# Performance work log

Hardware: AMD Instinct MI355X
Metric: run time of the kernel (lower is better)

Reference implementation:

```python
import jax, jax.numpy as jnp
import numpy as np
from jax import lax

FS, DW, CIN, COUT, NCLS, BATCH = 128, 8, 64, 256, 2, 512
K1, S1 = FS // 4, FS // 8          # 32, 16
L = FS * DW                        # 1024
T = (L - K1) // S1 + 1             # 63 SNN timesteps
BN_EPS = 1e-5


@jax.custom_vjp
def spike(u):
    """Heaviside spike on (v - threshold); surrogate grad exp(-|u|) (tau_grad=scale_grad=1)."""
    return (u >= 0).astype(u.dtype)

def _spike_fwd(u):
    return (u >= 0).astype(u.dtype), u

def _spike_bwd(u, g):
    return (g * jnp.exp(-jnp.abs(u)),)

spike.defvjp(_spike_fwd, _spike_bwd)


def cuba(x, threshold, current_decay, voltage_decay):
    """CUBA LIF scan. x: [N,C,T] -> binary spikes [N,C,T].
    i[t] = (1-cd)*i[t-1] + x[t]; v[t] = (1-vd)*v[t-1] + i[t]; s = v>=theta; v *= (1-s)."""
    cd, vd = 1.0 - current_decay, 1.0 - voltage_decay
    xs = jnp.moveaxis(x, -1, 0)  # [T,N,C]
    zero = jnp.zeros(x.shape[:-1], x.dtype)

    def step(carry, xt):
        i, v = carry
        i = cd * i + xt
        v = vd * v + i
        s = spike(v - threshold)
        v = v * (1.0 - s)
        return (i, v), s

    _, s = lax.scan(step, (zero, zero), xs)
    return jnp.moveaxis(s, 0, -1)


def conv1d(x, w, b, stride, pad):
    y = lax.conv_general_dilated(x, w, (stride,), [(pad, pad)],
                                 dimension_numbers=('NCH', 'OIH', 'NCH'))
    return y + b[None, :, None]


def bn(x, g, b, m, v):
    scale = g / jnp.sqrt(v + BN_EPS)
    return (x - m[None, :, None]) * scale[None, :, None] + b[None, :, None]


def setup_inputs() -> dict:
    key = jax.random.key(0)
    ks = jax.random.split(key, 12)
    return {
        'x':       jax.random.normal(ks[0], (BATCH, CIN, L), jnp.float32),
        'conv1_w': jax.random.normal(ks[1], (COUT, CIN, K1), jnp.float32) * 0.05,
        'conv1_b': jax.random.normal(ks[2], (COUT,), jnp.float32) * 0.05,
        'bn1_g':   jax.random.uniform(ks[3], (COUT,), jnp.float32, 0.5, 1.5),
        'bn1_b':   jax.random.normal(ks[4], (COUT,), jnp.float32) * 0.1,
        'bn1_m':   jax.random.normal(ks[5], (COUT,), jnp.float32) * 0.1,
        'bn1_v':   jax.random.uniform(ks[6], (COUT,), jnp.float32, 0.5, 1.5),
        'conv2_w': jax.random.normal(ks[7], (COUT, COUT, 3), jnp.float32) * 0.05,
        'conv2_b': jax.random.normal(ks[8], (COUT,), jnp.float32) * 0.05,
        'bn2_g':   jax.random.uniform(ks[9], (COUT,), jnp.float32, 0.5, 1.5),
        'bn2_b':   jax.random.normal(ks[10], (COUT,), jnp.float32) * 0.1,
        'bn2_m':   jax.random.normal(ks[11], (COUT,), jnp.float32) * 0.1,
        'bn2_v':   jax.random.uniform(jax.random.fold_in(key, 100), (COUT,), jnp.float32, 0.5, 1.5),
        'w1':      jax.random.normal(jax.random.fold_in(key, 101), (COUT, COUT), jnp.float32) * 0.1,
        'w2':      jax.random.normal(jax.random.fold_in(key, 102), (NCLS, COUT), jnp.float32) * 0.1,
    }


def reference(x, conv1_w, conv1_b, bn1_g, bn1_b, bn1_m, bn1_v,
              conv2_w, conv2_b, bn2_g, bn2_b, bn2_m, bn2_v, w1, w2):
    # CNN frontend (eval mode: BN uses running stats, dropout is identity)
    z = bn(conv1d(x, conv1_w, conv1_b, S1, 0), bn1_g, bn1_b, bn1_m, bn1_v)   # [N,COUT,T]
    z = bn(conv1d(z, conv2_w, conv2_b, 1, 1), bn2_g, bn2_b, bn2_m, bn2_v)    # [N,COUT,T]
    # CUBA Input encoder block: threshold=0.3, current_decay=0.9, voltage_decay=0.9
    z = cuba(z, 0.3, 0.9, 0.9)
    # CUBA Dense blocks (bias-free synapse per timestep + LIF): threshold=0.1, cd=1, vd=0.1
    z = cuba(jnp.einsum('oc,nct->not', w1, z), 0.1, 1.0, 0.1)
    z = cuba(jnp.einsum('oc,nct->not', w2, z), 0.1, 1.0, 0.1)
    return z  # binary spike trains [N, n_classes, T]
```

## Files before the change

kernel.cpp:

```cpp
#include <hip/hip_runtime.h>
#include <cstdint>
#include <cstddef>


typedef _Float16 half8 __attribute__((ext_vector_type(8)));
typedef float floatx4 __attribute__((ext_vector_type(4)));

__device__ __forceinline__ void split_f32(float v, _Float16& hi, _Float16& lo) {
    _Float16 h = (_Float16)v;
    hi = h;
    lo = (_Float16)((v - (float)h) * 2048.0f);
}

__global__ __launch_bounds__(256) void prep_kernel(
    const float* __restrict__ c1w, const float* __restrict__ c1b,
    const float* __restrict__ g1,  const float* __restrict__ b1,
    const float* __restrict__ m1,  const float* __restrict__ v1,
    const float* __restrict__ c2w, const float* __restrict__ c2b,
    const float* __restrict__ g2,  const float* __restrict__ b2,
    const float* __restrict__ m2,  const float* __restrict__ v2,
    const float* __restrict__ w1,
    _Float16* __restrict__ w1h, _Float16* __restrict__ w1l,
    _Float16* __restrict__ w2h, _Float16* __restrict__ w2l,
    _Float16* __restrict__ wdh, _Float16* __restrict__ wdl,
    float* __restrict__ ab1, float* __restrict__ ab2)
{
    const int id = blockIdx.x * 256 + threadIdx.x;
    if (id < 256) {
        float a1 = g1[id] / sqrtf(v1[id] + 1e-5f);
        ab1[id]       = a1;
        ab1[256 + id] = (c1b[id] - m1[id]) * a1 + b1[id];
        float a2 = g2[id] / sqrtf(v2[id] + 1e-5f);
        ab2[id]       = a2;
        ab2[256 + id] = (c2b[id] - m2[id]) * a2 + b2[id];
    }
    split_f32(w1[id], wdh[id], wdl[id]);
    for (int idx = id; idx < 256 * 2048; idx += 65536)
        split_f32(c1w[idx], w1h[idx], w1l[idx]);
    for (int idx = id; idx < 256 * 768; idx += 65536) {
        const int o  = idx / 768;
        const int r  = idx - o * 768;
        const int dt = r >> 8;
        const int c  = r & 255;
        split_f32(c2w[o * 768 + c * 3 + dt], w2h[idx], w2l[idx]);
    }
}

__global__ __launch_bounds__(256, 2) void conv1_mfma(
    const float* __restrict__ x,
    const _Float16* __restrict__ w1h, const _Float16* __restrict__ w1l,
    const float* __restrict__ ab,
    _Float16* __restrict__ z1h, _Float16* __restrict__ z1l)
{
    __shared__ _Float16 Ah[4][128][8];
    __shared__ _Float16 Al[4][128][8];
    __shared__ _Float16 Bh[4][128][8];
    __shared__ _Float16 Bl[4][128][8];

    const int tid = threadIdx.x;
    const int bm = blockIdx.x, bn = blockIdx.y;
    const int lr = tid & 127;
    const int h  = tid >> 7;

    const int am = bm * 128 + lr;
    const int an = am / 63, at = am - an * 63;
    const float*    arow  = x   + (size_t)an * 65536 + at * 16 + h * 16;
    const _Float16* bhrow = w1h + (size_t)(bn * 128 + lr) * 2048 + h * 16;
    const _Float16* blrow = w1l + (size_t)(bn * 128 + lr) * 2048 + h * 16;

    const int lane = tid & 63;
    const int wv   = tid >> 6;
    const int mw   = wv & 1, nw = wv >> 1;
    const int quad = lane >> 4;
    const int l15  = lane & 15;

    floatx4 accA[4][4] = {};
    floatx4 accB[4][4] = {};

    for (int it = 0; it < 64; ++it) {
        const float* ap = arow + it * 1024;
        float va[16];
        *(float4*)&va[0]  = *(const float4*)(ap);
        *(float4*)&va[4]  = *(const float4*)(ap + 4);
        *(float4*)&va[8]  = *(const float4*)(ap + 8);
        *(float4*)&va[12] = *(const float4*)(ap + 12);
        int4 bh0 = *(const int4*)(bhrow + it * 32);
        int4 bh1 = *(const int4*)(bhrow + it * 32 + 8);
        int4 bl0 = *(const int4*)(blrow + it * 32);
        int4 bl1 = *(const int4*)(blrow + it * 32 + 8);

        union U { _Float16 hf[8]; int4 v; };
        U c0h, c0l, c1h, c1l;
#pragma unroll
        for (int j = 0; j < 8; ++j) split_f32(va[j],     c0h.hf[j], c0l.hf[j]);
#pragma unroll
        for (int j = 0; j < 8; ++j) split_f32(va[8 + j], c1h.hf[j], c1l.hf[j]);

        __syncthreads();
        *(int4*)&Ah[2*h  ][lr][0] = c0h.v;
        *(int4*)&Ah[2*h+1][lr][0] = c1h.v;
        *(int4*)&Al[2*h  ][lr][0] = c0l.v;
        *(int4*)&Al[2*h+1][lr][0] = c1l.v;
        *(int4*)&Bh[2*h  ][lr][0] = bh0;
        *(int4*)&Bh[2*h+1][lr][0] = bh1;
        *(int4*)&Bl[2*h  ][lr][0] = bl0;
        *(int4*)&Bl[2*h+1][lr][0] = bl1;
        __syncthreads();

        half8 fah[4], fal[4], fbh[4], fbl[4];
#pragma unroll
        for (int t = 0; t < 4; ++t) {
            fah[t] = *(const half8*)&Ah[quad][mw*64 + t*16 + l15][0];
            fal[t] = *(const half8*)&Al[quad][mw*64 + t*16 + l15][0];
            fbh[t] = *(const half8*)&Bh[quad][nw*64 + t*16 + l15][0];
            fbl[t] = *(const half8*)&Bl[quad][nw*64 + t*16 + l15][0];
        }
#pragma unroll
        for (int ti = 0; ti < 4; ++ti)
#pragma unroll
            for (int tj = 0; tj < 4; ++tj) {
                accA[ti][tj] = __builtin_amdgcn_mfma_f32_16x16x32_f16(fah[ti], fbh[tj], accA[ti][tj], 0, 0, 0);
                accB[ti][tj] = __builtin_amdgcn_mfma_f32_16x16x32_f16(fah[ti], fbl[tj], accB[ti][tj], 0, 0, 0);
                accB[ti][tj] = __builtin_amdgcn_mfma_f32_16x16x32_f16(fal[ti], fbh[tj], accB[ti][tj], 0, 0, 0);
            }
    }

#pragma unroll
    for (int tj = 0; tj < 4; ++tj) {
        const int o = bn*128 + nw*64 + tj*16 + l15;
        const float alpha = ab[o], beta = ab[256 + o];
#pragma unroll
        for (int ti = 0; ti < 4; ++ti) {
            const int m0 = bm*128 + mw*64 + ti*16 + quad*4;
#pragma unroll
            for (int r = 0; r < 4; ++r) {
                float c = accA[ti][tj][r] + accB[ti][tj][r] * (1.0f/2048.0f);
                float z = c * alpha + beta;
                _Float16 zh, zl;
                split_f32(z, zh, zl);
                const size_t off = (size_t)(m0 + r) * 256 + o;
                z1h[off] = zh;
                z1l[off] = zl;
            }
        }
    }
}

__global__ __launch_bounds__(256, 2) void conv2_mfma(
    const _Float16* __restrict__ z1h, const _Float16* __restrict__ z1l,
    const _Float16* __restrict__ w2h, const _Float16* __restrict__ w2l,
    const float* __restrict__ ab, float* __restrict__ z2)
{
    __shared__ _Float16 Ah[4][128][8];
    __shared__ _Float16 Al[4][128][8];
    __shared__ _Float16 Bh[4][128][8];
    __shared__ _Float16 Bl[4][128][8];

    const int tid = threadIdx.x;
    const int bm = blockIdx.x, bn = blockIdx.y;
    const int lr = tid & 127;
    const int h  = tid >> 7;

    const int am = bm * 128 + lr;
    const int an = am / 63, at = am - an * 63;
    const _Float16* abase_h = z1h + (size_t)an * 16128;
    const _Float16* abase_l = z1l + (size_t)an * 16128;
    const _Float16* bhrow = w2h + (size_t)(bn * 128 + lr) * 768 + h * 16;
    const _Float16* blrow = w2l + (size_t)(bn * 128 + lr) * 768 + h * 16;

    const int lane = tid & 63;
    const int wv   = tid >> 6;
    const int mw   = wv & 1, nw = wv >> 1;
    const int quad = lane >> 4;
    const int l15  = lane & 15;

    floatx4 accA[4][4] = {};
    floatx4 accB[4][4] = {};

    const int4 z4 = {0, 0, 0, 0};

    for (int it = 0; it < 24; ++it) {
        const int kap0 = it * 32;
        const int dt   = kap0 >> 8;
        const int c0   = kap0 & 255;
        const int trow = at + dt - 1;
        const bool valid = (trow >= 0) && (trow < 63);
        const _Float16* aph = abase_h + trow * 256 + c0 + h * 16;
        const _Float16* apl = abase_l + trow * 256 + c0 + h * 16;
        int4 a0h = valid ? *(const int4*)(aph)     : z4;
        int4 a1h = valid ? *(const int4*)(aph + 8) : z4;
        int4 a0l = valid ? *(const int4*)(apl)     : z4;
        int4 a1l = valid ? *(const int4*)(apl + 8) : z4;
        int4 b0h = *(const int4*)(bhrow + kap0);
        int4 b1h = *(const int4*)(bhrow + kap0 + 8);
        int4 b0l = *(const int4*)(blrow + kap0);
        int4 b1l = *(const int4*)(blrow + kap0 + 8);

        __syncthreads();
        *(int4*)&Ah[2*h  ][lr][0] = a0h;
        *(int4*)&Ah[2*h+1][lr][0] = a1h;
        *(int4*)&Al[2*h  ][lr][0] = a0l;
        *(int4*)&Al[2*h+1][lr][0] = a1l;
        *(int4*)&Bh[2*h  ][lr][0] = b0h;
        *(int4*)&Bh[2*h+1][lr][0] = b1h;
        *(int4*)&Bl[2*h  ][lr][0] = b0l;
        *(int4*)&Bl[2*h+1][lr][0] = b1l;
        __syncthreads();

        half8 fah[4], fal[4], fbh[4], fbl[4];
#pragma unroll
        for (int t = 0; t < 4; ++t) {
            fah[t] = *(const half8*)&Ah[quad][mw*64 + t*16 + l15][0];
            fal[t] = *(const half8*)&Al[quad][mw*64 + t*16 + l15][0];
            fbh[t] = *(const half8*)&Bh[quad][nw*64 + t*16 + l15][0];
            fbl[t] = *(const half8*)&Bl[quad][nw*64 + t*16 + l15][0];
        }
#pragma unroll
        for (int ti = 0; ti < 4; ++ti)
#pragma unroll
            for (int tj = 0; tj < 4; ++tj) {
                accA[ti][tj] = __builtin_amdgcn_mfma_f32_16x16x32_f16(fah[ti], fbh[tj], accA[ti][tj], 0, 0, 0);
                accB[ti][tj] = __builtin_amdgcn_mfma_f32_16x16x32_f16(fah[ti], fbl[tj], accB[ti][tj], 0, 0, 0);
                accB[ti][tj] = __builtin_amdgcn_mfma_f32_16x16x32_f16(fal[ti], fbh[tj], accB[ti][tj], 0, 0, 0);
            }
    }

#pragma unroll
    for (int tj = 0; tj < 4; ++tj) {
        const int o = bn*128 + nw*64 + tj*16 + l15;
        const float alpha = ab[o], beta = ab[256 + o];
#pragma unroll
        for (int ti = 0; ti < 4; ++ti) {
            const int m0 = bm*128 + mw*64 + ti*16 + quad*4;
#pragma unroll
            for (int r = 0; r < 4; ++r) {
                float c = accA[ti][tj][r] + accB[ti][tj][r] * (1.0f/2048.0f);
                z2[(size_t)(m0 + r) * 256 + o] = c * alpha + beta;
            }
        }
    }
}

__global__ __launch_bounds__(256) void cuba1_kernel(
    const float* __restrict__ z2, _Float16* __restrict__ s1)
{
    const int n   = blockIdx.x;
    const int tid = threadIdx.x;
    const float* zrow = z2 + (size_t)n * 16128 + tid;
    _Float16*    srow = s1 + (size_t)n * 16128 + tid;
    float cur = 0.f, vol = 0.f;
    for (int t = 0; t < 63; ++t) {
        float xv = zrow[(size_t)t * 256];
        cur = 0.1f * cur + xv;
        vol = 0.1f * vol + cur;
        bool sp = (vol - 0.3f) >= 0.f;
        srow[(size_t)t * 256] = sp ? (_Float16)1.0f : (_Float16)0.0f;
        if (sp) vol = 0.f;
    }
}

__global__ __launch_bounds__(256, 2) void dense1_mfma(
    const _Float16* __restrict__ s1,
    const _Float16* __restrict__ wdh, const _Float16* __restrict__ wdl,
    float* __restrict__ y1)
{
    __shared__ _Float16 As[4][128][8];
    __shared__ _Float16 Bh[4][128][8];
    __shared__ _Float16 Bl[4][128][8];

    const int tid = threadIdx.x;
    const int bm = blockIdx.x, bn = blockIdx.y;
    const int lr = tid & 127;
    const int h  = tid >> 7;

    const _Float16* arow  = s1  + (size_t)(bm * 128 + lr) * 256 + h * 16;
    const _Float16* bhrow = wdh + (size_t)(bn * 128 + lr) * 256 + h * 16;
    const _Float16* blrow = wdl + (size_t)(bn * 128 + lr) * 256 + h * 16;

    const int lane = tid & 63;
    const int wv   = tid >> 6;
    const int mw   = wv & 1, nw = wv >> 1;
    const int quad = lane >> 4;
    const int l15  = lane & 15;

    floatx4 accA[4][4] = {};
    floatx4 accB[4][4] = {};

    for (int it = 0; it < 8; ++it) {
        const int kap0 = it * 32;
        int4 a0 = *(const int4*)(arow + kap0);
        int4 a1 = *(const int4*)(arow + kap0 + 8);
        int4 b0h = *(const int4*)(bhrow + kap0);
        int4 b1h = *(const int4*)(bhrow + kap0 + 8);
        int4 b0l = *(const int4*)(blrow + kap0);
        int4 b1l = *(const int4*)(blrow + kap0 + 8);

        __syncthreads();
        *(int4*)&As[2*h  ][lr][0] = a0;
        *(int4*)&As[2*h+1][lr][0] = a1;
        *(int4*)&Bh[2*h  ][lr][0] = b0h;
        *(int4*)&Bh[2*h+1][lr][0] = b1h;
        *(int4*)&Bl[2*h  ][lr][0] = b0l;
        *(int4*)&Bl[2*h+1][lr][0] = b1l;
        __syncthreads();

        half8 fa[4], fbh[4], fbl[4];
#pragma unroll
        for (int t = 0; t < 4; ++t) {
            fa[t]  = *(const half8*)&As[quad][mw*64 + t*16 + l15][0];
            fbh[t] = *(const half8*)&Bh[quad][nw*64 + t*16 + l15][0];
            fbl[t] = *(const half8*)&Bl[quad][nw*64 + t*16 + l15][0];
        }
#pragma unroll
        for (int ti = 0; ti < 4; ++ti)
#pragma unroll
            for (int tj = 0; tj < 4; ++tj) {
                accA[ti][tj] = __builtin_amdgcn_mfma_f32_16x16x32_f16(fa[ti], fbh[tj], accA[ti][tj], 0, 0, 0);
                accB[ti][tj] = __builtin_amdgcn_mfma_f32_16x16x32_f16(fa[ti], fbl[tj], accB[ti][tj], 0, 0, 0);
            }
    }

#pragma unroll
    for (int tj = 0; tj < 4; ++tj) {
        const int o = bn*128 + nw*64 + tj*16 + l15;
#pragma unroll
        for (int ti = 0; ti < 4; ++ti) {
            const int m0 = bm*128 + mw*64 + ti*16 + quad*4;
#pragma unroll
            for (int r = 0; r < 4; ++r)
                y1[(size_t)(m0 + r) * 256 + o] =
                    accA[ti][tj][r] + accB[ti][tj][r] * (1.0f/2048.0f);
        }
    }
}

__global__ __launch_bounds__(256) void snn_tail(
    const float* __restrict__ y1, const float* __restrict__ w2,
    float* __restrict__ out)
{
    __shared__ unsigned long long M2[256];
    __shared__ float Y[2 * 63];
    const int n   = blockIdx.x;
    const int tid = threadIdx.x;

    {
        const float* yrow = y1 + (size_t)n * 16128 + tid;
        float v = 0.f;
        unsigned long long mask2 = 0ull;
        for (int t = 0; t < 63; ++t) {
            float yv = yrow[(size_t)t * 256];
            v = 0.9f * v + yv;
            if ((v - 0.1f) >= 0.f) { mask2 |= (1ull << t); v = 0.f; }
        }
        M2[tid] = mask2;
    }
    __syncthreads();

    if (tid < 126) {
        const int cls = tid / 63;
        const int t   = tid - cls * 63;
        const float* wrow = w2 + cls * 256;
        float acc = 0.f;
#pragma unroll 4
        for (int o = 0; o < 256; ++o)
            acc += ((M2[o] >> t) & 1ull) ? wrow[o] : 0.f;
        Y[cls * 63 + t] = acc;
    }
    __syncthreads();
    if (tid < 2) {
        float v = 0.f;
        float* orow = out + (size_t)n * 126 + tid * 63;
        for (int t = 0; t < 63; ++t) {
            v = 0.9f * v + Y[tid * 63 + t];
            float u = v - 0.1f;
            float s = (u >= 0.f) ? 1.f : 0.f;
            orow[t] = s;
            v = (u >= 0.f) ? 0.f : v;
        }
    }
}

extern "C" void kernel_launch(void* const* d_in, const int* in_sizes, int n_in,
                              void* d_out, int out_size, void* d_ws, size_t ws_size,
                              hipStream_t stream)
{
    const float* x    = (const float*)d_in[0];
    const float* c1w  = (const float*)d_in[1];
    const float* c1b  = (const float*)d_in[2];
    const float* g1   = (const float*)d_in[3];
    const float* b1   = (const float*)d_in[4];
    const float* m1   = (const float*)d_in[5];
    const float* v1   = (const float*)d_in[6];
    const float* c2w  = (const float*)d_in[7];
    const float* c2b  = (const float*)d_in[8];
    const float* g2   = (const float*)d_in[9];
    const float* b2   = (const float*)d_in[10];
    const float* m2   = (const float*)d_in[11];
    const float* v2   = (const float*)d_in[12];
    const float* w1   = (const float*)d_in[13];
    const float* w2   = (const float*)d_in[14];
    float* out = (float*)d_out;

    float* ws = (float*)d_ws;
    float*    zA  = ws;
    _Float16* z1h = (_Float16*)zA;
    _Float16* z1l = (_Float16*)(zA + 4128768);
    float*    y1  = zA;
    float*    z2  = zA + 8257536;
    _Float16* s1  = (_Float16*)(z2 + 8257536);
    float*    wsp = z2 + 8257536 + 4128768;
    _Float16* w1h = (_Float16*)wsp;
    _Float16* w1l = (_Float16*)(wsp + 262144);
    _Float16* w2h = (_Float16*)(wsp + 2*262144);
    _Float16* w2l = (_Float16*)(wsp + 2*262144 + 98304);
    _Float16* wdh = (_Float16*)(wsp + 2*262144 + 2*98304);
    _Float16* wdl = (_Float16*)(wsp + 2*262144 + 2*98304 + 32768);
    float*    ab1 = wsp + 2*262144 + 2*98304 + 2*32768;
    float*    ab2 = ab1 + 512;

    prep_kernel<<<256, 256, 0, stream>>>(c1w, c1b, g1, b1, m1, v1,
                                         c2w, c2b, g2, b2, m2, v2,
                                         w1, w1h, w1l, w2h, w2l, wdh, wdl,
                                         ab1, ab2);
    conv1_mfma<<<dim3(252, 2), 256, 0, stream>>>(x, w1h, w1l, ab1, z1h, z1l);
    conv2_mfma<<<dim3(252, 2), 256, 0, stream>>>(z1h, z1l, w2h, w2l, ab2, z2);
    cuba1_kernel<<<512, 256, 0, stream>>>(z2, s1);
    dense1_mfma<<<dim3(252, 2), 256, 0, stream>>>(s1, wdh, wdl, y1);
    snn_tail<<<512, 256, 0, stream>>>(y1, w2, out);
}
```

Baseline: 434.3 us.

## Double-buffer LDS tiles and use direct global-to-LDS loads in GEMM kernels

Converts the conv1, conv2 and dense1 MFMA kernels to double-buffered shared-memory tiles. The next K-slice is prefetched while MFMAs run on the current one, which removes one of the two barriers per iteration. Weight (and dense1 activation) tiles are loaded with global_load_lds DMA straight into LDS instead of going through registers. This doubles LDS use per block, and correctness depends on the DMA completing before the single barrier, which may need explicit vmcnt waits.

```diff
diff --git a/kernel.cpp b/kernel.cpp
--- a/kernel.cpp
+++ b/kernel.cpp
@@ -10,6 +10,12 @@
     _Float16 h = (_Float16)v;
     hi = h;
     lo = (_Float16)((v - (float)h) * 2048.0f);
+}
+
+typedef const __attribute__((address_space(1))) unsigned int* gas_ptr;
+typedef __attribute__((address_space(3))) unsigned int* las_ptr;
+__device__ __forceinline__ void lds_dma16(const void* g, void* l) {
+    __builtin_amdgcn_global_load_lds((gas_ptr)g, (las_ptr)l, 16, 0, 0);
 }
 
 __global__ __launch_bounds__(256) void prep_kernel(
@@ -52,10 +58,10 @@
     const float* __restrict__ ab,
     _Float16* __restrict__ z1h, _Float16* __restrict__ z1l)
 {
-    __shared__ _Float16 Ah[4][128][8];
-    __shared__ _Float16 Al[4][128][8];
-    __shared__ _Float16 Bh[4][128][8];
-    __shared__ _Float16 Bl[4][128][8];
+    __shared__ _Float16 Ah[2][4][128][8];
+    __shared__ _Float16 Al[2][4][128][8];
+    __shared__ _Float16 Bh[2][4][128][8];
+    __shared__ _Float16 Bl[2][4][128][8];
 
     const int tid = threadIdx.x;
     const int bm = blockIdx.x, bn = blockIdx.y;
@@ -64,9 +70,7 @@
 
     const int am = bm * 128 + lr;
     const int an = am / 63, at = am - an * 63;
-    const float*    arow  = x   + (size_t)an * 65536 + at * 16 + h * 16;
-    const _Float16* bhrow = w1h + (size_t)(bn * 128 + lr) * 2048 + h * 16;
-    const _Float16* blrow = w1l + (size_t)(bn * 128 + lr) * 2048 + h * 16;
+    const float* arow = x + (size_t)an * 65536 + at * 16 + h * 16;
 
     const int lane = tid & 63;
     const int wv   = tid >> 6;
@@ -74,46 +78,63 @@
     const int quad = lane >> 4;
     const int l15  = lane & 15;
 
+    const int q0 = wv >> 1;
+    const int rh = (wv & 1) * 64;
+    const _Float16* bh_g = w1h + (size_t)(bn * 128 + rh + lane) * 2048;
+    const _Float16* bl_g = w1l + (size_t)(bn * 128 + rh + lane) * 2048;
+
     floatx4 accA[4][4] = {};
     floatx4 accB[4][4] = {};
 
+    union U { _Float16 hf[8]; int4 v; };
+    float va[16];
+
+    {
+        *(float4*)&va[0]  = *(const float4*)(arow);
+        *(float4*)&va[4]  = *(const float4*)(arow + 4);
+        *(float4*)&va[8]  = *(const float4*)(arow + 8);
+        *(float4*)&va[12] = *(const float4*)(arow + 12);
+        lds_dma16(bh_g + q0 * 8,       &Bh[0][q0    ][rh][0]);
+        lds_dma16(bh_g + (q0 + 2) * 8, &Bh[0][q0 + 2][rh][0]);
+        lds_dma16(bl_g + q0 * 8,       &Bl[0][q0    ][rh][0]);
+        lds_dma16(bl_g + (q0 + 2) * 8, &Bl[0][q0 + 2][rh][0]);
+        U c0h, c0l, c1h, c1l;
+#pragma unroll
+        for (int j = 0; j < 8; ++j) split_f32(va[j],     c0h.hf[j], c0l.hf[j]);
+#pragma unroll
+        for (int j = 0; j < 8; ++j) split_f32(va[8 + j], c1h.hf[j], c1l.hf[j]);
+        *(int4*)&Ah[0][2*h  ][lr][0] = c0h.v;
+        *(int4*)&Ah[0][2*h+1][lr][0] = c1h.v;
+        *(int4*)&Al[0][2*h  ][lr][0] = c0l.v;
+        *(int4*)&Al[0][2*h+1][lr][0] = c1l.v;
+        __syncthreads();
+    }
+
+    int cur = 0;
     for (int it = 0; it < 64; ++it) {
-        const float* ap = arow + it * 1024;
-        float va[16];
-        *(float4*)&va[0]  = *(const float4*)(ap);
-        *(float4*)&va[4]  = *(const float4*)(ap + 4);
-        *(float4*)&va[8]  = *(const float4*)(ap + 8);
-        *(float4*)&va[12] = *(const float4*)(ap + 12);
-        int4 bh0 = *(const int4*)(bhrow + it * 32);
-        int4 bh1 = *(const int4*)(bhrow + it * 32 + 8);
-        int4 bl0 = *(const int4*)(blrow + it * 32);
-        int4 bl1 = *(const int4*)(blrow + it * 32 + 8);
-
-        union U { _Float16 hf[8]; int4 v; };
-        U c0h, c0l, c1h, c1l;
-#pragma unroll
-        for (int j = 0; j < 8; ++j) split_f32(va[j],     c0h.hf[j], c0l.hf[j]);
-#pragma unroll
-        for (int j = 0; j < 8; ++j) split_f32(va[8 + j], c1h.hf[j], c1l.hf[j]);
-
-        __syncthreads();
-        *(int4*)&Ah[2*h  ][lr][0] = c0h.v;
-        *(int4*)&Ah[2*h+1][lr][0] = c1h.v;
-        *(int4*)&Al[2*h  ][lr][0] = c0l.v;
-        *(int4*)&Al[2*h+1][lr][0] = c1l.v;
-        *(int4*)&Bh[2*h  ][lr][0] = bh0;
-        *(int4*)&Bh[2*h+1][lr][0] = bh1;
-        *(int4*)&Bl[2*h  ][lr][0] = bl0;
-        *(int4*)&Bl[2*h+1][lr][0] = bl1;
-        __syncthreads();
+        const int nxt = cur ^ 1;
+        const bool pf = (it < 63);
+
+        if (pf) {
+            const float* ap = arow + (it + 1) * 1024;
+            *(float4*)&va[0]  = *(const float4*)(ap);
+            *(float4*)&va[4]  = *(const float4*)(ap + 4);
+            *(float4*)&va[8]  = *(const float4*)(ap + 8);
+            *(float4*)&va[12] = *(const float4*)(ap + 12);
+            const int ko = (it + 1) * 32;
+            lds_dma16(bh_g + ko + q0 * 8,       &Bh[nxt][q0    ][rh][0]);
+            lds_dma16(bh_g + ko + (q0 + 2) * 8, &Bh[nxt][q0 + 2][rh][0]);
+            lds_dma16(bl_g + ko + q0 * 8,       &Bl[nxt][q0    ][rh][0]);
+            lds_dma16(bl_g + ko + (q0 + 2) * 8, &Bl[nxt][q0 + 2][rh][0]);
+        }
 
         half8 fah[4], fal[4], fbh[4], fbl[4];
 #pragma unroll
         for (int t = 0; t < 4; ++t) {
-            fah[t] = *(const half8*)&Ah[quad][mw*64 + t*16 + l15][0];
-            fal[t] = *(const half8*)&Al[quad][mw*64 + t*16 + l15][0];
-            fbh[t] = *(const half8*)&Bh[quad][nw*64 + t*16 + l15][0];
-            fbl[t] = *(const half8*)&Bl[quad][nw*64 + t*16 + l15][0];
+            fah[t] = *(const half8*)&Ah[cur][quad][mw*64 + t*16 + l15][0];
+            fal[t] = *(const half8*)&Al[cur][quad][mw*64 + t*16 + l15][0];
+            fbh[t] = *(const half8*)&Bh[cur][quad][nw*64 + t*16 + l15][0];
+            fbl[t] = *(const half8*)&Bl[cur][quad][nw*64 + t*16 + l15][0];
         }
 #pragma unroll
         for (int ti = 0; ti < 4; ++ti)
@@ -123,6 +144,20 @@
                 accB[ti][tj] = __builtin_amdgcn_mfma_f32_16x16x32_f16(fah[ti], fbl[tj], accB[ti][tj], 0, 0, 0);
                 accB[ti][tj] = __builtin_amdgcn_mfma_f32_16x16x32_f16(fal[ti], fbh[tj], accB[ti][tj], 0, 0, 0);
             }
+
+        if (pf) {
+            U c0h, c0l, c1h, c1l;
+#pragma unroll
+            for (int j = 0; j < 8; ++j) split_f32(va[j],     c0h.hf[j], c0l.hf[j]);
+#pragma unroll
+            for (int j = 0; j < 8; ++j) split_f32(va[8 + j], c1h.hf[j], c1l.hf[j]);
+            *(int4*)&Ah[nxt][2*h  ][lr][0] = c0h.v;
+            *(int4*)&Ah[nxt][2*h+1][lr][0] = c1h.v;
+            *(int4*)&Al[nxt][2*h  ][lr][0] = c0l.v;
+            *(int4*)&Al[nxt][2*h+1][lr][0] = c1l.v;
+        }
+        __syncthreads();
+        cur = nxt;
     }
 
 #pragma unroll
@@ -151,10 +186,10 @@
     const _Float16* __restrict__ w2h, const _Float16* __restrict__ w2l,
     const float* __restrict__ ab, float* __restrict__ z2)
 {
-    __shared__ _Float16 Ah[4][128][8];
-    __shared__ _Float16 Al[4][128][8];
-    __shared__ _Float16 Bh[4][128][8];
-    __shared__ _Float16 Bl[4][128][8];
+    __shared__ _Float16 Ah[2][4][128][8];
+    __shared__ _Float16 Al[2][4][128][8];
+    __shared__ _Float16 Bh[2][4][128][8];
+    __shared__ _Float16 Bl[2][4][128][8];
 
     const int tid = threadIdx.x;
     const int bm = blockIdx.x, bn = blockIdx.y;
@@ -165,8 +200,6 @@
     const int an = am / 63, at = am - an * 63;
     const _Float16* abase_h = z1h + (size_t)an * 16128;
     const _Float16* abase_l = z1l + (size_t)an * 16128;
-    const _Float16* bhrow = w2h + (size_t)(bn * 128 + lr) * 768 + h * 16;
-    const _Float16* blrow = w2l + (size_t)(bn * 128 + lr) * 768 + h * 16;
 
     const int lane = tid & 63;
     const int wv   = tid >> 6;
@@ -174,12 +207,18 @@
     const int quad = lane >> 4;
     const int l15  = lane & 15;
 
+    const int q0 = wv >> 1;
+    const int rh = (wv & 1) * 64;
+    const _Float16* bh_g = w2h + (size_t)(bn * 128 + rh + lane) * 768;
+    const _Float16* bl_g = w2l + (size_t)(bn * 128 + rh + lane) * 768;
+
     floatx4 accA[4][4] = {};
     floatx4 accB[4][4] = {};
 
     const int4 z4 = {0, 0, 0, 0};
-
-    for (int it = 0; it < 24; ++it) {
+    int4 a0h, a1h, a0l, a1l;
+
+    auto loadA = [&](int it, int4& r0h, int4& r1h, int4& r0l, int4& r1l) {
         const int kap0 = it * 32;
         const int dt   = kap0 >> 8;
         const int c0   = kap0 & 255;
@@ -187,33 +226,46 @@
         const bool valid = (trow >= 0) && (trow < 63);
         const _Float16* aph = abase_h + trow * 256 + c0 + h * 16;
         const _Float16* apl = abase_l + trow * 256 + c0 + h * 16;
-        int4 a0h = valid ? *(const int4*)(aph)     : z4;
-        int4 a1h = valid ? *(const int4*)(aph + 8) : z4;
-        int4 a0l = valid ? *(const int4*)(apl)     : z4;
-        int4 a1l = valid ? *(const int4*)(apl + 8) : z4;
-        int4 b0h = *(const int4*)(bhrow + kap0);
-        int4 b1h = *(const int4*)(bhrow + kap0 + 8);
-        int4 b0l = *(const int4*)(blrow + kap0);
-        int4 b1l = *(const int4*)(blrow + kap0 + 8);
-
+        r0h = valid ? *(const int4*)(aph)     : z4;
+        r1h = valid ? *(const int4*)(aph + 8) : z4;
+        r0l = valid ? *(const int4*)(apl)     : z4;
+        r1l = valid ? *(const int4*)(apl + 8) : z4;
+    };
+
+    {
+        loadA(0, a0h, a1h, a0l, a1l);
+        lds_dma16(bh_g + q0 * 8,       &Bh[0][q0    ][rh][0]);
+        lds_dma16(bh_g + (q0 + 2) * 8, &Bh[0][q0 + 2][rh][0]);
+        lds_dma16(bl_g + q0 * 8,       &Bl[0][q0    ][rh][0]);
+        lds_dma16(bl_g + (q0 + 2) * 8, &Bl[0][q0 + 2][rh][0]);
+        *(int4*)&Ah[0][2*h  ][lr][0] = a0h;
+        *(int4*)&Ah[0][2*h+1][lr][0] = a1h;
+        *(int4*)&Al[0][2*h  ][lr][0] = a0l;
+        *(int4*)&Al[0][2*h+1][lr][0] = a1l;
         __syncthreads();
-        *(int4*)&Ah[2*h  ][lr][0] = a0h;
-        *(int4*)&Ah[2*h+1][lr][0] = a1h;
-        *(int4*)&Al[2*h  ][lr][0] = a0l;
-        *(int4*)&Al[2*h+1][lr][0] = a1l;
-        *(int4*)&Bh[2*h  ][lr][0] = b0h;
-        *(int4*)&Bh[2*h+1][lr][0] = b1h;
-        *(int4*)&Bl[2*h  ][lr][0] = b0l;
-        *(int4*)&Bl[2*h+1][lr][0] = b1l;
-        __syncthreads();
+    }
+
+    int cur = 0;
+    for (int it = 0; it < 24; ++it) {
+        const int nxt = cur ^ 1;
+        const bool pf = (it < 23);
+
+        if (pf) {
+            loadA(it + 1, a0h, a1h, a0l, a1l);
+            const int ko = (it + 1) * 32;
+            lds_dma16(bh_g + ko + q0 * 8,       &Bh[nxt][q0    ][rh][0]);
+            lds_dma16(bh_g + ko + (q0 + 2) * 8, &Bh[nxt][q0 + 2][rh][0]);
+            lds_dma16(bl_g + ko + q0 * 8,       &Bl[nxt][q0    ][rh][0]);
+            lds_dma16(bl_g + ko + (q0 + 2) * 8, &Bl[nxt][q0 + 2][rh][0]);
+        }
 
         half8 fah[4], fal[4], fbh[4], fbl[4];
 #pragma unroll
         for (int t = 0; t < 4; ++t) {
-            fah[t] = *(const half8*)&Ah[quad][mw*64 + t*16 + l15][0];
-            fal[t] = *(const half8*)&Al[quad][mw*64 + t*16 + l15][0];
-            fbh[t] = *(const half8*)&Bh[quad][nw*64 + t*16 + l15][0];
-            fbl[t] = *(const half8*)&Bl[quad][nw*64 + t*16 + l15][0];
+            fah[t] = *(const half8*)&Ah[cur][quad][mw*64 + t*16 + l15][0];
+            fal[t] = *(const half8*)&Al[cur][quad][mw*64 + t*16 + l15][0];
+            fbh[t] = *(const half8*)&Bh[cur][quad][nw*64 + t*16 + l15][0];
+            fbl[t] = *(const half8*)&Bl[cur][quad][nw*64 + t*16 + l15][0];
         }
 #pragma unroll
         for (int ti = 0; ti < 4; ++ti)
@@ -223,6 +275,15 @@
                 accB[ti][tj] = __builtin_amdgcn_mfma_f32_16x16x32_f16(fah[ti], fbl[tj], accB[ti][tj], 0, 0, 0);
                 accB[ti][tj] = __builtin_amdgcn_mfma_f32_16x16x32_f16(fal[ti], fbh[tj], accB[ti][tj], 0, 0, 0);
             }
+
+        if (pf) {
+            *(int4*)&Ah[nxt][2*h  ][lr][0] = a0h;
+            *(int4*)&Ah[nxt][2*h+1][lr][0] = a1h;
+            *(int4*)&Al[nxt][2*h  ][lr][0] = a0l;
+            *(int4*)&Al[nxt][2*h+1][lr][0] = a1l;
+        }
+        __syncthreads();
+        cur = nxt;
     }
 
 #pragma unroll
@@ -264,18 +325,12 @@
     const _Float16* __restrict__ wdh, const _Float16* __restrict__ wdl,
     float* __restrict__ y1)
 {
-    __shared__ _Float16 As[4][128][8];
-    __shared__ _Float16 Bh[4][128][8];
-    __shared__ _Float16 Bl[4][128][8];
+    __shared__ _Float16 As[2][4][128][8];
+    __shared__ _Float16 Bh[2][4][128][8];
+    __shared__ _Float16 Bl[2][4][128][8];
 
     const int tid = threadIdx.x;
     const int bm = blockIdx.x, bn = blockIdx.y;
-    const int lr = tid & 127;
-    const int h  = tid >> 7;
-
-    const _Float16* arow  = s1  + (size_t)(bm * 128 + lr) * 256 + h * 16;
-    const _Float16* bhrow = wdh + (size_t)(bn * 128 + lr) * 256 + h * 16;
-    const _Float16* blrow = wdl + (size_t)(bn * 128 + lr) * 256 + h * 16;
 
     const int lane = tid & 63;
     const int wv   = tid >> 6;
@@ -283,33 +338,46 @@
     const int quad = lane >> 4;
     const int l15  = lane & 15;
 
+    const int q0 = wv >> 1;
+    const int rh = (wv & 1) * 64;
+    const _Float16* a_g  = s1  + (size_t)(bm * 128 + rh + lane) * 256;
+    const _Float16* bh_g = wdh + (size_t)(bn * 128 + rh + lane) * 256;
+    const _Float16* bl_g = wdl + (size_t)(bn * 128 + rh + lane) * 256;
+
     floatx4 accA[4][4] = {};
     floatx4 accB[4][4] = {};
 
+    {
+        lds_dma16(a_g  + q0 * 8,       &As[0][q0    ][rh][0]);
+        lds_dma16(a_g  + (q0 + 2) * 8, &As[0][q0 + 2][rh][0]);
+        lds_dma16(bh_g + q0 * 8,       &Bh[0][q0    ][rh][0]);
+        lds_dma16(bh_g + (q0 + 2) * 8, &Bh[0][q0 + 2][rh][0]);
+        lds_dma16(bl_g + q0 * 8,       &Bl[0][q0    ][rh][0]);
+        lds_dma16(bl_g + (q0 + 2) * 8, &Bl[0][q0 + 2][rh][0]);
+        __syncthreads();
+    }
+
+    int cur = 0;
     for (int it = 0; it < 8; ++it) {
-        const int kap0 = it * 32;
-        int4 a0 = *(const int4*)(arow + kap0);
-        int4 a1 = *(const int4*)(arow + kap0 + 8);
-        int4 b0h = *(const int4*)(bhrow + kap0);
-        int4 b1h = *(const int4*)(bhrow + kap0 + 8);
-        int4 b0l = *(const int4*)(blrow + kap0);
-        int4 b1l = *(const int4*)(blrow + kap0 + 8);
-
-        __syncthreads();
-        *(int4*)&As[2*h  ][lr][0] = a0;
-        *(int4*)&As[2*h+1][lr][0] = a1;
-        *(int4*)&Bh[2*h  ][lr][0] = b0h;
-        *(int4*)&Bh[2*h+1][lr][0] = b1h;
-        *(int4*)&Bl[2*h  ][lr][0] = b0l;
-        *(int4*)&Bl[2*h+1][lr][0] = b1l;
-        __syncthreads();
+        const int nxt = cur ^ 1;
+        const bool pf = (it < 7);
+
+        if (pf) {
+            const int ko = (it + 1) * 32;
+            lds_dma16(a_g  + ko + q0 * 8,       &As[nxt][q0    ][rh][0]);
+            lds_dma16(a_g  + ko + (q0 + 2) * 8, &As[nxt][q0 + 2][rh][0]);
+            lds_dma16(bh_g + ko + q0 * 8,       &Bh[nxt][q0    ][rh][0]);
+            lds_dma16(bh_g + ko + (q0 + 2) * 8, &Bh[nxt][q0 + 2][rh][0]);
+            lds_dma16(bl_g + ko + q0 * 8,       &Bl[nxt][q0    ][rh][0]);
+            lds_dma16(bl_g + ko + (q0 + 2) * 8, &Bl[nxt][q0 + 2][rh][0]);
+        }
 
         half8 fa[4], fbh[4], fbl[4];
 #pragma unroll
         for (int t = 0; t < 4; ++t) {
-            fa[t]  = *(const half8*)&As[quad][mw*64 + t*16 + l15][0];
-            fbh[t] = *(const half8*)&Bh[quad][nw*64 + t*16 + l15][0];
-            fbl[t] = *(const half8*)&Bl[quad][nw*64 + t*16 + l15][0];
+            fa[t]  = *(const half8*)&As[cur][quad][mw*64 + t*16 + l15][0];
+            fbh[t] = *(const half8*)&Bh[cur][quad][nw*64 + t*16 + l15][0];
+            fbl[t] = *(const half8*)&Bl[cur][quad][nw*64 + t*16 + l15][0];
         }
 #pragma unroll
         for (int ti = 0; ti < 4; ++ti)
@@ -318,6 +386,9 @@
                 accA[ti][tj] = __builtin_amdgcn_mfma_f32_16x16x32_f16(fa[ti], fbh[tj], accA[ti][tj], 0, 0, 0);
                 accB[ti][tj] = __builtin_amdgcn_mfma_f32_16x16x32_f16(fa[ti], fbl[tj], accB[ti][tj], 0, 0, 0);
             }
+
+        __syncthreads();
+        cur = nxt;
     }
 
 #pragma unroll
```

Result: slower. 449.7 us (+3.5%).

## Pad conv1 output in time and stage conv2/dense1 tiles via global-to-LDS DMA

Applied to the files above, without the earlier changes.

Conv1 now writes its output into a time-padded layout with zeroed halo rows, and prep_kernel clears those halo rows. Conv2 can then drop its boundary checks and treat the k=3 conv as a contiguous K walk. Conv2 and dense1 load their A/B tiles with global_load_lds, which copies straight from global memory into LDS and skips the register round trip. They also take K=64 per barrier pair instead of 32, which halves the number of syncs at the cost of doubling shared memory. The cuba1 scan is unrolled in chunks of 9 so that loads are batched ahead of the serial recurrence.

```diff
diff --git a/kernel.cpp b/kernel.cpp
--- a/kernel.cpp
+++ b/kernel.cpp
@@ -10,6 +10,12 @@
     _Float16 h = (_Float16)v;
     hi = h;
     lo = (_Float16)((v - (float)h) * 2048.0f);
+}
+
+typedef const __attribute__((address_space(1))) unsigned int* gas_ptr;
+typedef __attribute__((address_space(3))) unsigned int* las_ptr;
+__device__ __forceinline__ void lds_dma16(const void* g, void* l) {
+    __builtin_amdgcn_global_load_lds((gas_ptr)g, (las_ptr)l, 16, 0, 0);
 }
 
 __global__ __launch_bounds__(256) void prep_kernel(
@@ -23,6 +29,7 @@
     _Float16* __restrict__ w1h, _Float16* __restrict__ w1l,
     _Float16* __restrict__ w2h, _Float16* __restrict__ w2l,
     _Float16* __restrict__ wdh, _Float16* __restrict__ wdl,
+    _Float16* __restrict__ z1ph, _Float16* __restrict__ z1pl,
     float* __restrict__ ab1, float* __restrict__ ab2)
 {
     const int id = blockIdx.x * 256 + threadIdx.x;
@@ -33,6 +40,16 @@
         float a2 = g2[id] / sqrtf(v2[id] + 1e-5f);
         ab2[id]       = a2;
         ab2[256 + id] = (c2b[id] - m2[id]) * a2 + b2[id];
+    }
+    {
+        const int n  = id >> 7;
+        const int j  = id & 127;
+        const int row = (j < 64) ? 0 : 64;
+        const int c0  = (j & 63) * 4;
+        const size_t off = ((size_t)n * 65 + row) * 256 + c0;
+        short4 zz = {0, 0, 0, 0};
+        *(short4*)&z1ph[off] = zz;
+        *(short4*)&z1pl[off] = zz;
     }
     split_f32(w1[id], wdh[id], wdl[id]);
     for (int idx = id; idx < 256 * 2048; idx += 65536)
@@ -50,7 +67,7 @@
     const float* __restrict__ x,
     const _Float16* __restrict__ w1h, const _Float16* __restrict__ w1l,
     const float* __restrict__ ab,
-    _Float16* __restrict__ z1h, _Float16* __restrict__ z1l)
+    _Float16* __restrict__ z1ph, _Float16* __restrict__ z1pl)
 {
     __shared__ _Float16 Ah[4][128][8];
     __shared__ _Float16 Al[4][128][8];
@@ -138,23 +155,26 @@
                 float z = c * alpha + beta;
                 _Float16 zh, zl;
                 split_f32(z, zh, zl);
-                const size_t off = (size_t)(m0 + r) * 256 + o;
-                z1h[off] = zh;
-                z1l[off] = zl;
+                const int m  = m0 + r;
+                const int a2 = m / 63;
+                const int t2 = m - a2 * 63;
+                const size_t off = ((size_t)a2 * 65 + t2 + 1) * 256 + o;
+                z1ph[off] = zh;
+                z1pl[off] = zl;
             }
         }
     }
 }
 
 __global__ __launch_bounds__(256, 2) void conv2_mfma(
-    const _Float16* __restrict__ z1h, const _Float16* __restrict__ z1l,
+    const _Float16* __restrict__ z1ph, const _Float16* __restrict__ z1pl,
     const _Float16* __restrict__ w2h, const _Float16* __restrict__ w2l,
     const float* __restrict__ ab, float* __restrict__ z2)
 {
-    __shared__ _Float16 Ah[4][128][8];
-    __shared__ _Float16 Al[4][128][8];
-    __shared__ _Float16 Bh[4][128][8];
-    __shared__ _Float16 Bl[4][128][8];
+    __shared__ _Float16 Ah[8][128][8];
+    __shared__ _Float16 Al[8][128][8];
+    __shared__ _Float16 Bh[8][128][8];
+    __shared__ _Float16 Bl[8][128][8];
 
     const int tid = threadIdx.x;
     const int bm = blockIdx.x, bn = blockIdx.y;
@@ -163,10 +183,10 @@
 
     const int am = bm * 128 + lr;
     const int an = am / 63, at = am - an * 63;
-    const _Float16* abase_h = z1h + (size_t)an * 16128;
-    const _Float16* abase_l = z1l + (size_t)an * 16128;
-    const _Float16* bhrow = w2h + (size_t)(bn * 128 + lr) * 768 + h * 16;
-    const _Float16* blrow = w2l + (size_t)(bn * 128 + lr) * 768 + h * 16;
+    const _Float16* pAh = z1ph + (size_t)an * 16640 + at * 256 + h * 8;
+    const _Float16* pAl = z1pl + (size_t)an * 16640 + at * 256 + h * 8;
+    const _Float16* pBh = w2h + (size_t)(bn * 128 + lr) * 768 + h * 8;
+    const _Float16* pBl = w2l + (size_t)(bn * 128 + lr) * 768 + h * 8;
 
     const int lane = tid & 63;
     const int wv   = tid >> 6;
@@ -177,52 +197,37 @@
     floatx4 accA[4][4] = {};
     floatx4 accB[4][4] = {};
 
-    const int4 z4 = {0, 0, 0, 0};
-
-    for (int it = 0; it < 24; ++it) {
-        const int kap0 = it * 32;
-        const int dt   = kap0 >> 8;
-        const int c0   = kap0 & 255;
-        const int trow = at + dt - 1;
-        const bool valid = (trow >= 0) && (trow < 63);
-        const _Float16* aph = abase_h + trow * 256 + c0 + h * 16;
-        const _Float16* apl = abase_l + trow * 256 + c0 + h * 16;
-        int4 a0h = valid ? *(const int4*)(aph)     : z4;
-        int4 a1h = valid ? *(const int4*)(aph + 8) : z4;
-        int4 a0l = valid ? *(const int4*)(apl)     : z4;
-        int4 a1l = valid ? *(const int4*)(apl + 8) : z4;
-        int4 b0h = *(const int4*)(bhrow + kap0);
-        int4 b1h = *(const int4*)(bhrow + kap0 + 8);
-        int4 b0l = *(const int4*)(blrow + kap0);
-        int4 b1l = *(const int4*)(blrow + kap0 + 8);
-
-        __syncthreads();
-        *(int4*)&Ah[2*h  ][lr][0] = a0h;
-        *(int4*)&Ah[2*h+1][lr][0] = a1h;
-        *(int4*)&Al[2*h  ][lr][0] = a0l;
-        *(int4*)&Al[2*h+1][lr][0] = a1l;
-        *(int4*)&Bh[2*h  ][lr][0] = b0h;
-        *(int4*)&Bh[2*h+1][lr][0] = b1h;
-        *(int4*)&Bl[2*h  ][lr][0] = b0l;
-        *(int4*)&Bl[2*h+1][lr][0] = b1l;
-        __syncthreads();
-
-        half8 fah[4], fal[4], fbh[4], fbl[4];
-#pragma unroll
-        for (int t = 0; t < 4; ++t) {
-            fah[t] = *(const half8*)&Ah[quad][mw*64 + t*16 + l15][0];
-            fal[t] = *(const half8*)&Al[quad][mw*64 + t*16 + l15][0];
-            fbh[t] = *(const half8*)&Bh[quad][nw*64 + t*16 + l15][0];
-            fbl[t] = *(const half8*)&Bl[quad][nw*64 + t*16 + l15][0];
-        }
-#pragma unroll
-        for (int ti = 0; ti < 4; ++ti)
-#pragma unroll
-            for (int tj = 0; tj < 4; ++tj) {
-                accA[ti][tj] = __builtin_amdgcn_mfma_f32_16x16x32_f16(fah[ti], fbh[tj], accA[ti][tj], 0, 0, 0);
-                accB[ti][tj] = __builtin_amdgcn_mfma_f32_16x16x32_f16(fah[ti], fbl[tj], accB[ti][tj], 0, 0, 0);
-                accB[ti][tj] = __builtin_amdgcn_mfma_f32_16x16x32_f16(fal[ti], fbh[tj], accB[ti][tj], 0, 0, 0);
+    for (int it = 0; it < 12; ++it) {
+        __syncthreads();
+#pragma unroll
+        for (int q = 0; q < 4; ++q) {
+            lds_dma16(pAh + q * 16, &Ah[q*2 + h][lr][0]);
+            lds_dma16(pAl + q * 16, &Al[q*2 + h][lr][0]);
+            lds_dma16(pBh + q * 16, &Bh[q*2 + h][lr][0]);
+            lds_dma16(pBl + q * 16, &Bl[q*2 + h][lr][0]);
+        }
+        __syncthreads();
+
+#pragma unroll
+        for (int ks = 0; ks < 2; ++ks) {
+            half8 fah[4], fal[4], fbh[4], fbl[4];
+#pragma unroll
+            for (int t = 0; t < 4; ++t) {
+                fah[t] = *(const half8*)&Ah[ks*4 + quad][mw*64 + t*16 + l15][0];
+                fal[t] = *(const half8*)&Al[ks*4 + quad][mw*64 + t*16 + l15][0];
+                fbh[t] = *(const half8*)&Bh[ks*4 + quad][nw*64 + t*16 + l15][0];
+                fbl[t] = *(const half8*)&Bl[ks*4 + quad][nw*64 + t*16 + l15][0];
             }
+#pragma unroll
+            for (int ti = 0; ti < 4; ++ti)
+#pragma unroll
+                for (int tj = 0; tj < 4; ++tj) {
+                    accA[ti][tj] = __builtin_amdgcn_mfma_f32_16x16x32_f16(fah[ti], fbh[tj], accA[ti][tj], 0, 0, 0);
+                    accB[ti][tj] = __builtin_amdgcn_mfma_f32_16x16x32_f16(fah[ti], fbl[tj], accB[ti][tj], 0, 0, 0);
+                    accB[ti][tj] = __builtin_amdgcn_mfma_f32_16x16x32_f16(fal[ti], fbh[tj], accB[ti][tj], 0, 0, 0);
+                }
+        }
+        pAh += 64; pAl += 64; pBh += 64; pBl += 64;
     }
 
 #pragma unroll
@@ -249,13 +254,19 @@
     const float* zrow = z2 + (size_t)n * 16128 + tid;
     _Float16*    srow = s1 + (size_t)n * 16128 + tid;
     float cur = 0.f, vol = 0.f;
-    for (int t = 0; t < 63; ++t) {
-        float xv = zrow[(size_t)t * 256];
-        cur = 0.1f * cur + xv;
-        vol = 0.1f * vol + cur;
-        bool sp = (vol - 0.3f) >= 0.f;
-        srow[(size_t)t * 256] = sp ? (_Float16)1.0f : (_Float16)0.0f;
-        if (sp) vol = 0.f;
+    for (int tb = 0; tb < 63; tb += 9) {
+        float xv[9];
+#pragma unroll
+        for (int j = 0; j < 9; ++j)
+            xv[j] = zrow[(size_t)(tb + j) * 256];
+#pragma unroll
+        for (int j = 0; j < 9; ++j) {
+            cur = 0.1f * cur + xv[j];
+            vol = 0.1f * vol + cur;
+            bool sp = (vol - 0.3f) >= 0.f;
+            srow[(size_t)(tb + j) * 256] = sp ? (_Float16)1.0f : (_Float16)0.0f;
+            if (sp) vol = 0.f;
+        }
     }
 }
 
@@ -264,18 +275,18 @@
     const _Float16* __restrict__ wdh, const _Float16* __restrict__ wdl,
     float* __restrict__ y1)
 {
-    __shared__ _Float16 As[4][128][8];
-    __shared__ _Float16 Bh[4][128][8];
-    __shared__ _Float16 Bl[4][128][8];
+    __shared__ _Float16 As[8][128][8];
+    __shared__ _Float16 Bh[8][128][8];
+    __shared__ _Float16 Bl[8][128][8];
 
     const int tid = threadIdx.x;
     const int bm = blockIdx.x, bn = blockIdx.y;
     const int lr = tid & 127;
     const int h  = tid >> 7;
 
-    const _Float16* arow  = s1  + (size_t)(bm * 128 + lr) * 256 + h * 16;
-    const _Float16* bhrow = wdh + (size_t)(bn * 128 + lr) * 256 + h * 16;
-    const _Float16* blrow = wdl + (size_t)(bn * 128 + lr) * 256 + h * 16;
+    const _Float16* pA  = s1  + (size_t)(bm * 128 + lr) * 256 + h * 8;
+    const _Float16* pBh = wdh + (size_t)(bn * 128 + lr) * 256 + h * 8;
+    const _Float16* pBl = wdl + (size_t)(bn * 128 + lr) * 256 + h * 8;
 
     const int lane = tid & 63;
     const int wv   = tid >> 6;
@@ -286,38 +297,34 @@
     floatx4 accA[4][4] = {};
     floatx4 accB[4][4] = {};
 
-    for (int it = 0; it < 8; ++it) {
-        const int kap0 = it * 32;
-        int4 a0 = *(const int4*)(arow + kap0);
-        int4 a1 = *(const int4*)(arow + kap0 + 8);
-        int4 b0h = *(const int4*)(bhrow + kap0);
-        int4 b1h = *(const int4*)(bhrow + kap0 + 8);
-        int4 b0l = *(const int4*)(blrow + kap0);
-        int4 b1l = *(const int4*)(blrow + kap0 + 8);
-
-        __syncthreads();
-        *(int4*)&As[2*h  ][lr][0] = a0;
-        *(int4*)&As[2*h+1][lr][0] = a1;
-        *(int4*)&Bh[2*h  ][lr][0] = b0h;
-        *(int4*)&Bh[2*h+1][lr][0] = b1h;
-        *(int4*)&Bl[2*h  ][lr][0] = b0l;
-        *(int4*)&Bl[2*h+1][lr][0] = b1l;
-        __syncthreads();
-
-        half8 fa[4], fbh[4], fbl[4];
-#pragma unroll
-        for (int t = 0; t < 4; ++t) {
-            fa[t]  = *(const half8*)&As[quad][mw*64 + t*16 + l15][0];
-            fbh[t] = *(const half8*)&Bh[quad][nw*64 + t*16 + l15][0];
-            fbl[t] = *(const half8*)&Bl[quad][nw*64 + t*16 + l15][0];
-        }
-#pragma unroll
-        for (int ti = 0; ti < 4; ++ti)
-#pragma unroll
-            for (int tj = 0; tj < 4; ++tj) {
-                accA[ti][tj] = __builtin_amdgcn_mfma_f32_16x16x32_f16(fa[ti], fbh[tj], accA[ti][tj], 0, 0, 0);
-                accB[ti][tj] = __builtin_amdgcn_mfma_f32_16x16x32_f16(fa[ti], fbl[tj], accB[ti][tj], 0, 0, 0);
+    for (int it = 0; it < 4; ++it) {
+        __syncthreads();
+#pragma unroll
+        for (int q = 0; q < 4; ++q) {
+            lds_dma16(pA  + q * 16, &As[q*2 + h][lr][0]);
+            lds_dma16(pBh + q * 16, &Bh[q*2 + h][lr][0]);
+            lds_dma16(pBl + q * 16, &Bl[q*2 + h][lr][0]);
+        }
+        __syncthreads();
+
+#pragma unroll
+        for (int ks = 0; ks < 2; ++ks) {
+            half8 fa[4], fbh[4], fbl[4];
+#pragma unroll
+            for (int t = 0; t < 4; ++t) {
+                fa[t]  = *(const half8*)&As[ks*4 + quad][mw*64 + t*16 + l15][0];
+                fbh[t] = *(const half8*)&Bh[ks*4 + quad][nw*64 + t*16 + l15][0];
+                fbl[t] = *(const half8*)&Bl[ks*4 + quad][nw*64 + t*16 + l15][0];
             }
+#pragma unroll
+            for (int ti = 0; ti < 4; ++ti)
+#pragma unroll
+                for (int tj = 0; tj < 4; ++tj) {
+                    accA[ti][tj] = __builtin_amdgcn_mfma_f32_16x16x32_f16(fa[ti], fbh[tj], accA[ti][tj], 0, 0, 0);
+                    accB[ti][tj] = __builtin_amdgcn_mfma_f32_16x16x32_f16(fa[ti], fbl[tj], accB[ti][tj], 0, 0, 0);
+                }
+        }
+        pA += 64; pBh += 64; pBl += 64;
     }
 
 #pragma unroll
@@ -402,13 +409,12 @@
     float* out = (float*)d_out;
 
     float* ws = (float*)d_ws;
-    float*    zA  = ws;
-    _Float16* z1h = (_Float16*)zA;
-    _Float16* z1l = (_Float16*)(zA + 4128768);
-    float*    y1  = zA;
-    float*    z2  = zA + 8257536;
-    _Float16* s1  = (_Float16*)(z2 + 8257536);
-    float*    wsp = z2 + 8257536 + 4128768;
+    _Float16* z1ph = (_Float16*)ws;
+    _Float16* z1pl = (_Float16*)(ws + 4259840);
+    float*    y1   = ws;
+    float*    z2   = ws + 8519680;
+    _Float16* s1   = (_Float16*)(ws + 16777216);
+    float*    wsp  = ws + 20905984;
     _Float16* w1h = (_Float16*)wsp;
     _Float16* w1l = (_Float16*)(wsp + 262144);
     _Float16* w2h = (_Float16*)(wsp + 2*262144);
@@ -421,9 +427,9 @@
     prep_kernel<<<256, 256, 0, stream>>>(c1w, c1b, g1, b1, m1, v1,
                                          c2w, c2b, g2, b2, m2, v2,
                                          w1, w1h, w1l, w2h, w2l, wdh, wdl,
-                                         ab1, ab2);
-    conv1_mfma<<<dim3(252, 2), 256, 0, stream>>>(x, w1h, w1l, ab1, z1h, z1l);
-    conv2_mfma<<<dim3(252, 2), 256, 0, stream>>>(z1h, z1l, w2h, w2l, ab2, z2);
+                                         z1ph, z1pl, ab1, ab2);
+    conv1_mfma<<<dim3(252, 2), 256, 0, stream>>>(x, w1h, w1l, ab1, z1ph, z1pl);
+    conv2_mfma<<<dim3(252, 2), 256, 0, stream>>>(z1ph, z1pl, w2h, w2l, ab2, z2);
     cuba1_kernel<<<512, 256, 0, stream>>>(z2, s1);
     dense1_mfma<<<dim3(252, 2), 256, 0, stream>>>(s1, wdh, wdl, y1);
     snn_tail<<<512, 256, 0, stream>>>(y1, w2, out);
```

Result: slower. 446.7 us (+2.9%).
